# Kernel optimization log

Hardware: AMD Instinct MI355X
Metric: run time of the kernel (lower is better)

Reference implementation:

```python
import jax, jax.numpy as jnp
import numpy as np

D_MODEL = 1024
NUM_HEADS = 16
ROPE_THETA = 10000.0


def setup_inputs() -> dict:
    key = jax.random.key(0)
    ks = jax.random.split(key, 5)
    B, S, D = 4, 2048, D_MODEL
    scale = 1.0 / np.sqrt(D)
    return {
        "x": jax.random.normal(ks[0], (B, S, D), dtype=jnp.float32),
        "Wq": jax.random.normal(ks[1], (D, D), dtype=jnp.float32) * scale,
        "Wk": jax.random.normal(ks[2], (D, D), dtype=jnp.float32) * scale,
        "Wv": jax.random.normal(ks[3], (D, D), dtype=jnp.float32) * scale,
        "Wo": jax.random.normal(ks[4], (D, D), dtype=jnp.float32) * scale,
        "token_positions": jnp.arange(S, dtype=jnp.int32),
    }


def _rope(x, pos, theta=ROPE_THETA):
    # x: (b, h, s, d); interleaved-pair rotary embedding
    d = x.shape[-1]
    inv_freq = 1.0 / (theta ** (jnp.arange(0, d, 2, dtype=jnp.float32) / d))  # (d/2,)
    ang = pos.astype(jnp.float32)[:, None] * inv_freq[None, :]  # (s, d/2)
    cos, sin = jnp.cos(ang), jnp.sin(ang)
    x1, x2 = x[..., ::2], x[..., 1::2]
    out = jnp.stack([x1 * cos - x2 * sin, x1 * sin + x2 * cos], axis=-1)
    return out.reshape(x.shape)


def reference(x, Wq, Wk, Wv, Wo, token_positions):
    B, S, D = x.shape
    H = NUM_HEADS
    dh = D // H
    # torch nn.Linear(bias=False): y = x @ W.T
    q = jnp.einsum('bsd,ed->bse', x, Wq).reshape(B, S, H, dh).transpose(0, 2, 1, 3)
    k = jnp.einsum('bsd,ed->bse', x, Wk).reshape(B, S, H, dh).transpose(0, 2, 1, 3)
    v = jnp.einsum('bsd,ed->bse', x, Wv).reshape(B, S, H, dh).transpose(0, 2, 1, 3)
    q = _rope(q, token_positions)
    k = _rope(k, token_positions)
    scores = jnp.einsum('bhqd,bhkd->bhqk', q, k) / jnp.sqrt(jnp.array(dh, x.dtype))
    causal = jnp.tril(jnp.ones((S, S), dtype=bool))
    scores = jnp.where(causal, scores, jnp.array(-jnp.inf, scores.dtype))
    probs = jax.nn.softmax(scores, axis=-1)
    attn = jnp.einsum('bhqk,bhkd->bhqd', probs, v)  # (b, h, s, dh)
    attn = attn.transpose(0, 2, 1, 3).reshape(B, S, D)
    return jnp.einsum('bsd,ed->bse', attn, Wo)
```

## Files before the change

### kernel.cpp

```cpp
#include <hip/hip_runtime.h>
#include <hip/hip_bf16.h>
#include <stdint.h>

#define S_LEN 2048
#define BATCH 4
#define NH    16
#define DH    64
#define DM    1024
#define MTOT  (BATCH*S_LEN)

typedef short bf16x8 __attribute__((ext_vector_type(8)));
typedef float f32x4 __attribute__((ext_vector_type(4)));
typedef uint32_t u32x4 __attribute__((ext_vector_type(4)));

__device__ __forceinline__ uint16_t f2bf(float f) {
  union { float f; uint32_t i; } c; c.f = f;
  uint32_t r = c.i + 0x7fffu + ((c.i >> 16) & 1u);
  return (uint16_t)(r >> 16);
}
__device__ __forceinline__ float bf2f(uint16_t u) {
  union { uint32_t i; float f; } c; c.i = ((uint32_t)u) << 16; return c.f;
}

__device__ __forceinline__ uint32_t cvt_pk_bf16(float a, float b) {
  uint32_t r;
  asm("v_cvt_pk_bf16_f32 %0, %1, %2" : "=v"(r) : "v"(a), "v"(b));
  return r;
}

__device__ __forceinline__ void async_copy16(void* lds, const void* g) {
  __builtin_amdgcn_global_load_lds(
      (const __attribute__((address_space(1))) void*)g,
      (__attribute__((address_space(3))) void*)lds, 16, 0, 0);
}

__global__ __launch_bounds__(256) void cvt_f32_bf16(const float* __restrict__ in,
                                                    uint16_t* __restrict__ out, int n4) {
  int stride = gridDim.x * blockDim.x;
  for (int i = blockIdx.x * blockDim.x + threadIdx.x; i < n4; i += stride) {
    float4 v = ((const float4*)in)[i];
    ushort4 o;
    o.x = f2bf(v.x); o.y = f2bf(v.y); o.z = f2bf(v.z); o.w = f2bf(v.w);
    ((ushort4*)out)[i] = o;
  }
}

__global__ __launch_bounds__(256) void cvt_w4(const float* __restrict__ wq,
                                              const float* __restrict__ wk,
                                              const float* __restrict__ wv,
                                              const float* __restrict__ wo,
                                              uint16_t* __restrict__ out) {
  const int sel = blockIdx.y;
  const float* src = sel == 0 ? wq : sel == 1 ? wk : sel == 2 ? wv : wo;
  uint16_t* dst = out + (size_t)sel * DM * DM;
  const int n4 = DM * DM / 4;
  const int stride = gridDim.x * blockDim.x;
  for (int i = blockIdx.x * blockDim.x + threadIdx.x; i < n4; i += stride) {
    float4 v = ((const float4*)src)[i];
    ushort4 o;
    o.x = f2bf(v.x); o.y = f2bf(v.y); o.z = f2bf(v.z); o.w = f2bf(v.w);
    ((ushort4*)dst)[i] = o;
  }
}

template<int MODE>
__global__ __launch_bounds__(256) void gemm_bt(const uint16_t* __restrict__ A,
                                               const uint16_t* __restrict__ Bw,
                                               void* __restrict__ outp) {
  constexpr int K = DM;
  __shared__ uint16_t lA[128 * 32];
  __shared__ uint16_t lB[128 * 32];
  const int tid = threadIdx.x;
  const int w = tid >> 6, lane = tid & 63;
  const int l15 = lane & 15, lhi = lane >> 4;
  const int wr = w >> 1, wc = w & 1;

  const int nx = gridDim.x, nwg = nx * gridDim.y;
  const int flat = blockIdx.y * nx + blockIdx.x;
  const int wg = (flat & 7) * (nwg >> 3) + (flat >> 3);
  const int bm = (wg / nx) * 128, bn = (wg % nx) * 128;

  f32x4 acc[4][4] = {};

  for (int k0 = 0; k0 < K; k0 += 32) {
#pragma unroll
    for (int i = 0; i < 2; ++i) {
      const int row = (i * 256 + tid) >> 2;
      const int cb = (tid & 3) * 16;
      async_copy16((char*)lA + i * 4096 + w * 1024,
                   (const char*)A + ((size_t)(bm + row) * K + k0) * 2 + cb);
      async_copy16((char*)lB + i * 4096 + w * 1024,
                   (const char*)Bw + ((size_t)(bn + row) * K + k0) * 2 + cb);
    }
    __syncthreads();
    bf16x8 af[4], bfr[4];
#pragma unroll
    for (int mf = 0; mf < 4; ++mf)
      af[mf] = *(const bf16x8*)((const char*)lA + (wr * 64 + mf * 16 + l15) * 64 + lhi * 16);
#pragma unroll
    for (int nf = 0; nf < 4; ++nf)
      bfr[nf] = *(const bf16x8*)((const char*)lB + (wc * 64 + nf * 16 + l15) * 64 + lhi * 16);
#pragma unroll
    for (int mf = 0; mf < 4; ++mf)
#pragma unroll
      for (int nf = 0; nf < 4; ++nf)
        acc[mf][nf] = __builtin_amdgcn_mfma_f32_16x16x32_bf16(af[mf], bfr[nf], acc[mf][nf], 0, 0, 0);
    __syncthreads();
  }

  if (MODE == 0) {
    uint16_t* out = (uint16_t*)outp;
#pragma unroll
    for (int mf = 0; mf < 4; ++mf)
#pragma unroll
      for (int nf = 0; nf < 4; ++nf)
#pragma unroll
        for (int r = 0; r < 4; ++r) {
          const int m = bm + wr * 64 + mf * 16 + lhi * 4 + r;
          const int n = bn + wc * 64 + nf * 16 + l15;
          const int b = m >> 11, s = m & (S_LEN - 1);
          const int tsel = n >> 10, e = n & 1023;
          const int h = e >> 6, d = e & 63;
          out[(size_t)tsel * (MTOT * DM) +
              (((size_t)(b * NH + h) * S_LEN + s) << 6) + d] = f2bf(acc[mf][nf][r]);
        }
  } else {
    float* out = (float*)outp;
#pragma unroll
    for (int mf = 0; mf < 4; ++mf)
#pragma unroll
      for (int nf = 0; nf < 4; ++nf)
#pragma unroll
        for (int r = 0; r < 4; ++r) {
          const int m = bm + wr * 64 + mf * 16 + lhi * 4 + r;
          const int n = bn + wc * 64 + nf * 16 + l15;
          out[(size_t)m * DM + n] = acc[mf][nf][r];
        }
  }
}

__global__ __launch_bounds__(256) void rope_kernel(uint32_t* __restrict__ q,
                                                   uint32_t* __restrict__ k,
                                                   const int* __restrict__ pos) {
  const int total = BATCH * NH * S_LEN * 32;
  const float l2t = 13.287712379549449f;
  const float qsc = 0.18033688011112042f;
  const int stride = gridDim.x * blockDim.x;
  for (int idx = blockIdx.x * blockDim.x + threadIdx.x; idx < total; idx += stride) {
    const int i = idx & 31;
    const int s = (idx >> 5) & (S_LEN - 1);
    const float p = (float)pos[s];
    const float inv = __builtin_amdgcn_exp2f(-(float)i * (l2t * (1.0f / 32.0f)));
    const float ang = p * inv;
    const float sn = sinf(ang), cs = cosf(ang);
    {
      uint32_t u = q[idx];
      float x1 = bf2f((uint16_t)(u & 0xffffu));
      float x2 = bf2f((uint16_t)(u >> 16));
      q[idx] = (uint32_t)f2bf((x1 * cs - x2 * sn) * qsc) |
               ((uint32_t)f2bf((x1 * sn + x2 * cs) * qsc) << 16);
    }
    {
      uint32_t u = k[idx];
      float x1 = bf2f((uint16_t)(u & 0xffffu));
      float x2 = bf2f((uint16_t)(u >> 16));
      k[idx] = (uint32_t)f2bf(x1 * cs - x2 * sn) | ((uint32_t)f2bf(x1 * sn + x2 * cs) << 16);
    }
  }
}

__global__ __launch_bounds__(256) void transpose_v(const uint16_t* __restrict__ v,
                                                   uint16_t* __restrict__ vt) {
  __shared__ uint16_t t[64 * 65];
  const int bh = blockIdx.y, s0 = blockIdx.x * 64;
  const uint16_t* vb = v + (size_t)bh * S_LEN * 64 + (size_t)s0 * 64;
  uint16_t* ob = vt + (size_t)bh * 64 * S_LEN + s0;
  for (int o = threadIdx.x; o < 64 * 64; o += 256) {
    const int r = o >> 6, c = o & 63;
    t[c * 65 + r] = vb[(size_t)r * 64 + c];
  }
  __syncthreads();
  for (int o = threadIdx.x; o < 64 * 64; o += 256) {
    const int d = o >> 6, p = o & 63;
    const int sp = (p & 32) | (((p >> 2) & 3) << 3) | (((p >> 4) & 1) << 2) | (p & 3);
    ob[(size_t)d * S_LEN + sp] = t[d * 65 + p];
  }
}

__global__ __launch_bounds__(512, 4) void attn_kernel(const uint16_t* __restrict__ q,
                                                      const uint16_t* __restrict__ kk,
                                                      const uint16_t* __restrict__ vt,
                                                      uint16_t* __restrict__ o) {
  const int bh = blockIdx.y;
  const int p = blockIdx.x;
  const int tid = threadIdx.x;
  const int w = __builtin_amdgcn_readfirstlane(tid >> 6);
  const int lane = tid & 63;
  const int l15 = lane & 15, lhi = lane >> 4;
  const uint16_t* qb = q + (size_t)bh * S_LEN * DH;
  const uint16_t* kb = kk + (size_t)bh * S_LEN * DH;
  const uint16_t* vb = vt + (size_t)bh * DH * S_LEN;

  __shared__ uint16_t lK[2][128 * 64];
  __shared__ uint16_t lV[2][64 * 128];

  const int krow_l = lane >> 3;
  const int scK = (lane & 7) ^ krow_l;
  const int vrow_l = lane >> 4;

  auto stage = [&](int b, int t) {
    const int k0 = t * 128;
#pragma unroll
    for (int i = 0; i < 2; ++i) {
      const int krow = w * 16 + i * 8 + krow_l;
      async_copy16((char*)lK[b] + w * 2048 + i * 1024 + lane * 16,
                   (const char*)kb + ((size_t)(k0 + krow) * 64 + scK * 8) * 2);
      const int vd = w * 8 + i * 4 + vrow_l;
      const int scV = (lane & 15) ^ (vd & 15);
      async_copy16((char*)lV[b] + w * 2048 + i * 1024 + lane * 16,
                   (const char*)vb + ((size_t)vd * S_LEN + k0 + scV * 8) * 2);
    }
  };

  stage(0, 0);
  asm volatile("s_waitcnt vmcnt(0)" ::: "memory");
  __syncthreads();

  int cur = 0;
  const int b_out = bh >> 4, h_out = bh & 15;

  for (int s = 0; s < 2; ++s) {
    const int qtile = s ? p : (15 - p);
    const int q0 = qtile * 128 + w * 16;

    bf16x8 qf[2];
#pragma unroll
    for (int c = 0; c < 2; ++c)
      qf[c] = *(const bf16x8*)(qb + (size_t)(q0 + l15) * DH + c * 32 + lhi * 8);

    f32x4 oa[4] = {};
    float mr = -1e30f, lr = 0.f;

    const int nt = qtile + 1;
    for (int t = 0; t < nt; ++t) {
      if (t + 1 < nt) stage(cur ^ 1, t + 1);
      else if (s == 0) stage(cur ^ 1, 0);

      const bool diag = (t == qtile);
      const int fMf = diag ? w : 7;
      const int fE  = diag ? (w | 1) : 7;
      const int cE  = diag ? (w >> 1) : 3;

      f32x4 sf[8];
      __builtin_amdgcn_s_setprio(1);
#pragma unroll
      for (int f = 0; f < 8; ++f) {
        f32x4 z = {0.f, 0.f, 0.f, 0.f};
        if (f <= fMf) {
          const int kr = f * 16 + l15;
          const char* kbase = (const char*)lK[cur] + kr * 128;
          bf16x8 kf0 = *(const bf16x8*)(kbase + ((lhi ^ (kr & 7)) << 4));
          bf16x8 kf1 = *(const bf16x8*)(kbase + (((4 + lhi) ^ (kr & 7)) << 4));
          z = __builtin_amdgcn_mfma_f32_16x16x32_bf16(kf0, qf[0], z, 0, 0, 0);
          z = __builtin_amdgcn_mfma_f32_16x16x32_bf16(kf1, qf[1], z, 0, 0, 0);
        }
        sf[f] = z;
      }
      __builtin_amdgcn_s_setprio(0);

      if (diag) {
        const int qrow = q0 + l15;
        const int k0 = t * 128;
#pragma unroll
        for (int f = 0; f < 8; ++f)
          if (f <= fE)
#pragma unroll
            for (int r = 0; r < 4; ++r) {
              const int kv = k0 + f * 16 + lhi * 4 + r;
              if (kv > qrow) sf[f][r] = -1e30f;
            }
      }

      float pm = -1e30f;
#pragma unroll
      for (int f = 0; f < 8; ++f)
        if (f <= fE)
#pragma unroll
          for (int r = 0; r < 4; ++r) pm = fmaxf(pm, sf[f][r]);
      pm = fmaxf(pm, __shfl_xor(pm, 16));
      pm = fmaxf(pm, __shfl_xor(pm, 32));

      if (!__all(pm <= mr + 8.0f)) {
        const float mn = fmaxf(mr, pm);
        const float resc = __builtin_amdgcn_exp2f(mr - mn);
        mr = mn;
        lr *= resc;
#pragma unroll
        for (int r = 0; r < 4; ++r) {
          const float rb = __shfl(resc, (lhi << 2) + r);
#pragma unroll
          for (int df = 0; df < 4; ++df) oa[df][r] *= rb;
        }
      }

      float rs = 0.f;
#pragma unroll
      for (int f = 0; f < 8; ++f)
        if (f <= fE)
#pragma unroll
          for (int r = 0; r < 4; ++r) {
            const float pv = __builtin_amdgcn_exp2f(sf[f][r] - mr);
            sf[f][r] = pv;
            rs += pv;
          }
      rs += __shfl_xor(rs, 16);
      rs += __shfl_xor(rs, 32);
      lr += rs;

#pragma unroll
      for (int c = 0; c < 4; ++c) {
        if (c <= cE) {
          u32x4 u;
          u.x = cvt_pk_bf16(sf[2 * c][0], sf[2 * c][1]);
          u.y = cvt_pk_bf16(sf[2 * c][2], sf[2 * c][3]);
          u.z = cvt_pk_bf16(sf[2 * c + 1][0], sf[2 * c + 1][1]);
          u.w = cvt_pk_bf16(sf[2 * c + 1][2], sf[2 * c + 1][3]);
          bf16x8 pa = __builtin_bit_cast(bf16x8, u);
          __builtin_amdgcn_s_setprio(1);
#pragma unroll
          for (int df = 0; df < 4; ++df) {
            const int vr = df * 16 + l15;
            bf16x8 vf = *(const bf16x8*)((const char*)lV[cur] + vr * 256 +
                                         ((((c << 2) + lhi) ^ (vr & 15)) << 4));
            oa[df] = __builtin_amdgcn_mfma_f32_16x16x32_bf16(pa, vf, oa[df], 0, 0, 0);
          }
          __builtin_amdgcn_s_setprio(0);
        }
      }

      asm volatile("s_waitcnt vmcnt(0)" ::: "memory");
      __syncthreads();
      cur ^= 1;
    }

    float inv[4];
#pragma unroll
    for (int r = 0; r < 4; ++r)
      inv[r] = __builtin_amdgcn_rcpf(__shfl(lr, (lhi << 2) + r));
#pragma unroll
    for (int df = 0; df < 4; ++df)
#pragma unroll
      for (int r = 0; r < 4; ++r) {
        const int srow_o = q0 + lhi * 4 + r;
        const float val = oa[df][r] * inv[r];
        const int d = df * 16 + l15;
        o[((size_t)(b_out * S_LEN + srow_o)) * DM + h_out * 64 + d] = f2bf(val);
      }
  }
}

extern "C" void kernel_launch(void* const* d_in, const int* in_sizes, int n_in,
                              void* d_out, int out_size, void* d_ws, size_t ws_size,
                              hipStream_t stream) {
  const float* x = (const float*)d_in[0];
  const float* Wq = (const float*)d_in[1];
  const float* Wk = (const float*)d_in[2];
  const float* Wv = (const float*)d_in[3];
  const float* Wo = (const float*)d_in[4];
  const int* pos = (const int*)d_in[5];

  char* ws = (char*)d_ws;
  size_t off = 0;
  auto alloc = [&](size_t bytes) {
    void* p = ws + off;
    off += (bytes + 255) & ~(size_t)255;
    return p;
  };
  uint16_t* xb    = (uint16_t*)alloc((size_t)MTOT * DM * 2);
  uint16_t* wqkvb = (uint16_t*)alloc((size_t)4 * DM * DM * 2);
  uint16_t* qkvb  = (uint16_t*)alloc((size_t)3 * MTOT * DM * 2);
  uint16_t* vtb   = (uint16_t*)alloc((size_t)MTOT * DM * 2);
  uint16_t* wob = wqkvb + (size_t)3 * DM * DM;
  uint16_t* qb = qkvb;
  uint16_t* kbuf = qkvb + (size_t)MTOT * DM;
  uint16_t* vbuf = qkvb + (size_t)2 * MTOT * DM;
  uint16_t* attnb = xb;

  cvt_f32_bf16<<<2048, 256, 0, stream>>>(x, xb, MTOT * DM / 4);
  cvt_w4<<<dim3(128, 4), 256, 0, stream>>>(Wq, Wk, Wv, Wo, wqkvb);

  gemm_bt<0><<<dim3(24, MTOT / 128), 256, 0, stream>>>(xb, wqkvb, qkvb);

  rope_kernel<<<2048, 256, 0, stream>>>((uint32_t*)qb, (uint32_t*)kbuf, pos);
  transpose_v<<<dim3(32, 64), 256, 0, stream>>>(vbuf, vtb);

  attn_kernel<<<dim3(8, 64), 512, 0, stream>>>(qb, kbuf, vtb, attnb);

  gemm_bt<1><<<dim3(8, MTOT / 128), 256, 0, stream>>>(attnb, wob, d_out);
}
```

Measured before the change: 186.9 us.

## Fuse V transpose into QKV GEMM epilogue and swizzle GEMM LDS layout

The QKV projection GEMM now writes the V slice directly into the transposed, permuted layout the attention kernel expects, using 4-wide stores. This removes the separate transpose_v kernel and its extra read and write of V. The GEMM's shared-memory tiles also gain an XOR swizzle on 16-byte chunks to reduce LDS bank conflicts on fragment loads. The V epilogue's strided stores may coalesce less well than the plain layout.

```diff
diff --git a/kernel.cpp b/kernel.cpp
--- a/kernel.cpp
+++ b/kernel.cpp
@@ -66,7 +66,8 @@
 template<int MODE>
 __global__ __launch_bounds__(256) void gemm_bt(const uint16_t* __restrict__ A,
                                                const uint16_t* __restrict__ Bw,
-                                               void* __restrict__ outp) {
+                                               void* __restrict__ outp,
+                                               uint16_t* __restrict__ vtp) {
   constexpr int K = DM;
   __shared__ uint16_t lA[128 * 32];
   __shared__ uint16_t lB[128 * 32];
@@ -86,7 +87,9 @@
 #pragma unroll
     for (int i = 0; i < 2; ++i) {
       const int row = (i * 256 + tid) >> 2;
-      const int cb = (tid & 3) * 16;
+      const int cc = tid & 3;
+      const int hr = (row ^ (row >> 2)) & 3;
+      const int cb = (cc ^ hr) * 16;
       async_copy16((char*)lA + i * 4096 + w * 1024,
                    (const char*)A + ((size_t)(bm + row) * K + k0) * 2 + cb);
       async_copy16((char*)lB + i * 4096 + w * 1024,
@@ -95,11 +98,17 @@
     __syncthreads();
     bf16x8 af[4], bfr[4];
 #pragma unroll
-    for (int mf = 0; mf < 4; ++mf)
-      af[mf] = *(const bf16x8*)((const char*)lA + (wr * 64 + mf * 16 + l15) * 64 + lhi * 16);
-#pragma unroll
-    for (int nf = 0; nf < 4; ++nf)
-      bfr[nf] = *(const bf16x8*)((const char*)lB + (wc * 64 + nf * 16 + l15) * 64 + lhi * 16);
+    for (int mf = 0; mf < 4; ++mf) {
+      const int ar = wr * 64 + mf * 16 + l15;
+      af[mf] = *(const bf16x8*)((const char*)lA + ar * 64 +
+                                ((lhi ^ ((ar ^ (ar >> 2)) & 3)) << 4));
+    }
+#pragma unroll
+    for (int nf = 0; nf < 4; ++nf) {
+      const int br = wc * 64 + nf * 16 + l15;
+      bfr[nf] = *(const bf16x8*)((const char*)lB + br * 64 +
+                                 ((lhi ^ ((br ^ (br >> 2)) & 3)) << 4));
+    }
 #pragma unroll
     for (int mf = 0; mf < 4; ++mf)
 #pragma unroll
@@ -109,21 +118,43 @@
   }
 
   if (MODE == 0) {
-    uint16_t* out = (uint16_t*)outp;
-#pragma unroll
-    for (int mf = 0; mf < 4; ++mf)
-#pragma unroll
-      for (int nf = 0; nf < 4; ++nf)
-#pragma unroll
-        for (int r = 0; r < 4; ++r) {
-          const int m = bm + wr * 64 + mf * 16 + lhi * 4 + r;
+    const int tsel = bn >> 10;
+    if (tsel < 2) {
+      uint16_t* out = (uint16_t*)outp + (size_t)tsel * ((size_t)MTOT * DM);
+#pragma unroll
+      for (int mf = 0; mf < 4; ++mf)
+#pragma unroll
+        for (int nf = 0; nf < 4; ++nf)
+#pragma unroll
+          for (int r = 0; r < 4; ++r) {
+            const int m = bm + wr * 64 + mf * 16 + lhi * 4 + r;
+            const int n = bn + wc * 64 + nf * 16 + l15;
+            const int b = m >> 11, s = m & (S_LEN - 1);
+            const int e = n & 1023;
+            const int h = e >> 6, d = e & 63;
+            out[(((size_t)(b * NH + h) * S_LEN + s) << 6) + d] = f2bf(acc[mf][nf][r]);
+          }
+    } else {
+#pragma unroll
+      for (int mf = 0; mf < 4; ++mf)
+#pragma unroll
+        for (int nf = 0; nf < 4; ++nf) {
+          const int m0 = bm + wr * 64 + mf * 16 + lhi * 4;
           const int n = bn + wc * 64 + nf * 16 + l15;
-          const int b = m >> 11, s = m & (S_LEN - 1);
-          const int tsel = n >> 10, e = n & 1023;
+          const int e = n & 1023;
           const int h = e >> 6, d = e & 63;
-          out[(size_t)tsel * (MTOT * DM) +
-              (((size_t)(b * NH + h) * S_LEN + s) << 6) + d] = f2bf(acc[mf][nf][r]);
+          const int b = m0 >> 11, s = m0 & (S_LEN - 1);
+          const int p0 = s & 63;
+          const int sp0 = (p0 & 32) | (((p0 >> 2) & 3) << 3) | (((p0 >> 4) & 1) << 2);
+          ushort4 u;
+          u.x = f2bf(acc[mf][nf][0]);
+          u.y = f2bf(acc[mf][nf][1]);
+          u.z = f2bf(acc[mf][nf][2]);
+          u.w = f2bf(acc[mf][nf][3]);
+          *(ushort4*)(vtp + ((size_t)(b * NH + h) * DH + d) * S_LEN +
+                      (s & ~63) + sp0) = u;
         }
+    }
   } else {
     float* out = (float*)outp;
 #pragma unroll
@@ -169,24 +200,6 @@
   }
 }
 
-__global__ __launch_bounds__(256) void transpose_v(const uint16_t* __restrict__ v,
-                                                   uint16_t* __restrict__ vt) {
-  __shared__ uint16_t t[64 * 65];
-  const int bh = blockIdx.y, s0 = blockIdx.x * 64;
-  const uint16_t* vb = v + (size_t)bh * S_LEN * 64 + (size_t)s0 * 64;
-  uint16_t* ob = vt + (size_t)bh * 64 * S_LEN + s0;
-  for (int o = threadIdx.x; o < 64 * 64; o += 256) {
-    const int r = o >> 6, c = o & 63;
-    t[c * 65 + r] = vb[(size_t)r * 64 + c];
-  }
-  __syncthreads();
-  for (int o = threadIdx.x; o < 64 * 64; o += 256) {
-    const int d = o >> 6, p = o & 63;
-    const int sp = (p & 32) | (((p >> 2) & 3) << 3) | (((p >> 4) & 1) << 2) | (p & 3);
-    ob[(size_t)d * S_LEN + sp] = t[d * 65 + p];
-  }
-}
-
 __global__ __launch_bounds__(512, 4) void attn_kernel(const uint16_t* __restrict__ q,
                                                       const uint16_t* __restrict__ kk,
                                                       const uint16_t* __restrict__ vt,
@@ -378,23 +391,21 @@
   };
   uint16_t* xb    = (uint16_t*)alloc((size_t)MTOT * DM * 2);
   uint16_t* wqkvb = (uint16_t*)alloc((size_t)4 * DM * DM * 2);
-  uint16_t* qkvb  = (uint16_t*)alloc((size_t)3 * MTOT * DM * 2);
+  uint16_t* qkb   = (uint16_t*)alloc((size_t)2 * MTOT * DM * 2);
   uint16_t* vtb   = (uint16_t*)alloc((size_t)MTOT * DM * 2);
   uint16_t* wob = wqkvb + (size_t)3 * DM * DM;
-  uint16_t* qb = qkvb;
-  uint16_t* kbuf = qkvb + (size_t)MTOT * DM;
-  uint16_t* vbuf = qkvb + (size_t)2 * MTOT * DM;
+  uint16_t* qb = qkb;
+  uint16_t* kbuf = qkb + (size_t)MTOT * DM;
   uint16_t* attnb = xb;
 
   cvt_f32_bf16<<<2048, 256, 0, stream>>>(x, xb, MTOT * DM / 4);
   cvt_w4<<<dim3(128, 4), 256, 0, stream>>>(Wq, Wk, Wv, Wo, wqkvb);
 
-  gemm_bt<0><<<dim3(24, MTOT / 128), 256, 0, stream>>>(xb, wqkvb, qkvb);
+  gemm_bt<0><<<dim3(24, MTOT / 128), 256, 0, stream>>>(xb, wqkvb, qkb, vtb);
 
   rope_kernel<<<2048, 256, 0, stream>>>((uint32_t*)qb, (uint32_t*)kbuf, pos);
-  transpose_v<<<dim3(32, 64), 256, 0, stream>>>(vbuf, vtb);
 
   attn_kernel<<<dim3(8, 64), 512, 0, stream>>>(qb, kbuf, vtb, attnb);
 
-  gemm_bt<1><<<dim3(8, MTOT / 128), 256, 0, stream>>>(attnb, wob, d_out);
-}
+  gemm_bt<1><<<dim3(8, MTOT / 128), 256, 0, stream>>>(attnb, wob, d_out, nullptr);
+}
```

New measurement: 188.3 us. About the same (+0.7%).
